# Performance work log

Hardware: AMD Instinct MI355X
Metric: run time of the kernel (lower is better)

Reference implementation:

```python
import jax, jax.numpy as jnp
import numpy as np

T, N, E = 4, 4096, 65536
XD, HD, ZD = 256, 256, 64
EPS = 1e-10


def setup_inputs() -> dict:
    key = jax.random.key(0)
    ks = jax.random.split(key, 30)
    rn = lambda k, sh, s=0.05: jax.random.normal(k, sh, dtype=jnp.float32) * s
    inp = {
        "x": rn(ks[0], (T, N, XD), 1.0),
        "edge_idx": jax.random.randint(ks[1], (T, 2, E), 0, N, dtype=jnp.int32),
        "adj": jax.random.bernoulli(ks[2], 0.005, (T, N, N)).astype(jnp.float32),
        "eps_noise": jax.random.normal(ks[3], (T, N, ZD), dtype=jnp.float32),
        "h0": jnp.zeros((1, N, HD), jnp.float32),
        # phi_x / phi_z (Linear+ReLU)
        "phi_x_w": rn(ks[4], (XD, HD)), "phi_x_b": jnp.zeros((HD,), jnp.float32),
        "phi_z_w": rn(ks[5], (ZD, HD)), "phi_z_b": jnp.zeros((HD,), jnp.float32),
        # encoder GCNs
        "enc_w": rn(ks[6], (2 * HD, HD)), "enc_b": jnp.zeros((HD,), jnp.float32),
        "enc_mean_w": rn(ks[7], (HD, ZD)), "enc_mean_b": jnp.zeros((ZD,), jnp.float32),
        "enc_std_w": rn(ks[8], (HD, ZD)), "enc_std_b": jnp.zeros((ZD,), jnp.float32),
        # prior MLPs
        "prior_w": rn(ks[9], (HD, HD)), "prior_b": jnp.zeros((HD,), jnp.float32),
        "prior_mean_w": rn(ks[10], (HD, ZD)), "prior_mean_b": jnp.zeros((ZD,), jnp.float32),
        "prior_std_w": rn(ks[11], (HD, ZD)), "prior_std_b": jnp.zeros((ZD,), jnp.float32),
        # graph-GRU GCNs (bias=False, n_layers=1; x-input is cat[phi_x, phi_z] -> 2*HD)
        "gru_xz_w": rn(ks[12], (2 * HD, HD)), "gru_hz_w": rn(ks[13], (HD, HD)),
        "gru_xr_w": rn(ks[14], (2 * HD, HD)), "gru_hr_w": rn(ks[15], (HD, HD)),
        "gru_xh_w": rn(ks[16], (2 * HD, HD)), "gru_hh_w": rn(ks[17], (HD, HD)),
    }
    return inp


def _gcn(xf, src, dst, W, b):
    """GCNConv: sym-normalized (A + I) aggregation, then bias. Returns pre-activation."""
    h = xf @ W                                             # [N, out]
    deg = 1.0 + jax.ops.segment_sum(jnp.ones(src.shape[0], xf.dtype), dst, num_segments=N)
    dinv = jax.lax.rsqrt(deg)                              # [N]
    norm = dinv[src] * dinv[dst]                           # [E]
    agg = jax.ops.segment_sum(h[src] * norm[:, None], dst, num_segments=N)
    agg = agg + (dinv * dinv)[:, None] * h                 # self-loop term
    if b is not None:
        agg = agg + b
    return agg


def reference(x, edge_idx, adj, eps_noise, h0,
              phi_x_w, phi_x_b, phi_z_w, phi_z_b,
              enc_w, enc_b, enc_mean_w, enc_mean_b, enc_std_w, enc_std_b,
              prior_w, prior_b, prior_mean_w, prior_mean_b, prior_std_w, prior_std_b,
              gru_xz_w, gru_hz_w, gru_xr_w, gru_hr_w, gru_xh_w, gru_hh_w):
    relu, sp, sig = jax.nn.relu, jax.nn.softplus, jax.nn.sigmoid
    h = h0                                                  # [1, N, HD]
    kld = jnp.float32(0.0)
    nll = jnp.float32(0.0)
    enc_means, prior_means = [], []
    nn_f = jnp.float32(N * N)
    for t in range(T):
        src, dst = edge_idx[t, 0], edge_idx[t, 1]
        phi_x_t = relu(x[t] @ phi_x_w + phi_x_b)                       # [N, HD]
        enc_in = jnp.concatenate([phi_x_t, h[-1]], axis=1)             # [N, 2HD]
        enc_t = relu(_gcn(enc_in, src, dst, enc_w, enc_b))
        enc_mean_t = _gcn(enc_t, src, dst, enc_mean_w, enc_mean_b)     # act = identity
        enc_std_t = sp(_gcn(enc_t, src, dst, enc_std_w, enc_std_b))
        prior_t = relu(h[-1] @ prior_w + prior_b)
        prior_mean_t = prior_t @ prior_mean_w + prior_mean_b
        prior_std_t = sp(prior_t @ prior_std_w + prior_std_b)
        z_t = eps_noise[t] * enc_std_t + enc_mean_t                    # reparameterize
        phi_z_t = relu(z_t @ phi_z_w + phi_z_b)
        dec_t = sig(z_t @ z_t.T)                                       # [N, N] decode
        # graph-GRU step (n_layers = 1, bias=False)
        gin = jnp.concatenate([phi_x_t, phi_z_t], axis=1)              # [N, 2HD]
        z_g = sig(_gcn(gin, src, dst, gru_xz_w, None) + _gcn(h[0], src, dst, gru_hz_w, None))
        r_g = sig(_gcn(gin, src, dst, gru_xr_w, None) + _gcn(h[0], src, dst, gru_hr_w, None))
        h_tilde = jnp.tanh(_gcn(gin, src, dst, gru_xh_w, None)
                           + _gcn(r_g * h[0], src, dst, gru_hh_w, None))
        h = (z_g * h[0] + (1.0 - z_g) * h_tilde)[None]                 # [1, N, HD]
        # KLD (faithful to _kld_gauss, including its sign convention)
        s1, s2 = enc_std_t + EPS, prior_std_t + EPS
        kld_el = (2.0 * jnp.log(s2) - 2.0 * jnp.log(s1)
                  - (s1 * s1 + (enc_mean_t - prior_mean_t) ** 2) / (s2 * s2) + 1.0)
        kld = kld + (0.5 / N) * jnp.mean(jnp.sum(kld_el, axis=0))
        # NLL (faithful quirk: BCE-with-logits applied to sigmoid output dec_t)
        a = adj[t]
        tsum = jnp.sum(a)
        posw = (nn_f - tsum) / tsum
        norm = nn_f / ((nn_f - tsum) * 2.0)
        bce = posw * a * sp(-dec_t) + (1.0 - a) * sp(dec_t)
        nll = nll + norm * jnp.mean(bce)
        enc_means.append(enc_mean_t)
        prior_means.append(prior_mean_t)
    return kld, nll, jnp.stack(enc_means), jnp.stack(prior_means), h
```

## Files before the change

kernel.cpp:

```cpp
#include <hip/hip_runtime.h>
#include <hip/hip_bf16.h>

#define T_STEPS 4
#define N 4096
#define E 65536
#define XD 256
#define HD 256
#define ZD 64

typedef __hip_bfloat16 bf16;
typedef __attribute__((ext_vector_type(8))) short short8;
typedef __attribute__((ext_vector_type(4))) float f32x4;

__device__ __forceinline__ float b2f(bf16 v){ return __bfloat162float(v); }
__device__ __forceinline__ bf16 f2b(float v){ return __float2bfloat16(v); }
__device__ __forceinline__ short f2s(float v){ return __builtin_bit_cast(short, f2b(v)); }
__device__ __forceinline__ float bits2f(unsigned int s){ return __builtin_bit_cast(float, s << 16); }
__device__ __forceinline__ float s2f(short s){ return bits2f((unsigned int)(unsigned short)s); }
__device__ __forceinline__ float splus(float x){ return (x > 15.f) ? x : __logf(1.f + __expf(x)); }
__device__ __forceinline__ float sigm(float x){ return 1.f/(1.f + __expf(-x)); }
__device__ __forceinline__ float ftanh(float x){ return 2.f/(1.f + __expf(-2.f*x)) - 1.f; }

__device__ __forceinline__ float ldI(const void* p, size_t i, int f){
  return f ? ((const float*)p)[i] : b2f(((const bf16*)p)[i]);
}
__device__ __forceinline__ void stO(void* p, size_t i, float v, int f){
  if (f) ((float*)p)[i] = v; else ((bf16*)p)[i] = f2b(v);
}
__device__ __forceinline__ void ld8b(const bf16* p, float v[8]){
  uint4 u = *(const uint4*)p;
  v[0]=bits2f(u.x & 0xffffu); v[1]=bits2f(u.x >> 16);
  v[2]=bits2f(u.y & 0xffffu); v[3]=bits2f(u.y >> 16);
  v[4]=bits2f(u.z & 0xffffu); v[5]=bits2f(u.z >> 16);
  v[6]=bits2f(u.w & 0xffffu); v[7]=bits2f(u.w >> 16);
}
__device__ __forceinline__ void ldW8(const void* W, size_t off, int f, float w[8]){
  if (f == 0){ ld8b((const bf16*)W + off, w); }
  else {
    const float* Wf = (const float*)W + off;
    float4 a = *(const float4*)Wf, b = *(const float4*)(Wf + 4);
    w[0]=a.x; w[1]=a.y; w[2]=a.z; w[3]=a.w; w[4]=b.x; w[5]=b.y; w[6]=b.z; w[7]=b.w;
  }
}
__device__ __forceinline__ unsigned int pack2(float a, float b){
  return (unsigned int)(unsigned short)__builtin_bit_cast(unsigned short, f2b(a))
       | ((unsigned int)(unsigned short)__builtin_bit_cast(unsigned short, f2b(b)) << 16);
}
__device__ __forceinline__ uint4 pack8(const float v[8]){
  uint4 o; o.x = pack2(v[0],v[1]); o.y = pack2(v[2],v[3]);
  o.z = pack2(v[4],v[5]); o.w = pack2(v[6],v[7]);
  return o;
}
__device__ __forceinline__ unsigned int pack2s(short a, short b){
  return (unsigned int)(unsigned short)a | ((unsigned int)(unsigned short)b << 16);
}
__device__ __forceinline__ const void* wofs(const void* W, int f, size_t elems){
  return f ? (const void*)((const float*)W + elems) : (const void*)((const bf16*)W + elems);
}

struct GemmSM { short As[64*72]; short Wt[64*72]; };
struct DecSM  { short Zi[64*72]; short Zj[64*72]; short Adj[64*72];
                float redA[256]; float redB[256]; float redC[256]; };
struct EncSM  { short At[16*264]; short Wt[128*40]; };

struct KP {
  const void *x, *adj, *eps, *h0;
  const int* ei;
  const void *phi_x_w, *phi_x_b, *phi_z_w, *phi_z_b;
  const void *enc_w, *enc_b, *enc_mean_w, *enc_mean_b, *enc_std_w, *enc_std_b;
  const void *prior_w, *prior_b, *prior_mean_w, *prior_mean_b, *prior_std_w, *prior_std_b;
  const void *gxz, *ghz, *gxr, *ghr, *gxh, *ghh;
  void* out;
  float* scal; int* dflag; float* dinv; int* offs; int* srcs; float* enorm; int* deg;
  float* h_prev; bf16* h_bf; bf16* phiXa; bf16* Tb1; bf16* Tb2;
  bf16* zbf; float* z_g; bf16* Gs1; bf16* Gsx; bf16* Gms; bf16* Gh2;
  bf16* PreB;
};

#define OUT_EM ((size_t)2)
#define OUT_PM ((size_t)(2 + (size_t)T_STEPS*N*ZD))
#define OUT_H  ((size_t)(2 + (size_t)2*T_STEPS*N*ZD))

__device__ void mfma_tile(GemmSM& sm, int tid, int f,
    const void* A, int am, int lda, int K,
    const void* W, int ldw, int wcol,
    const void* bias, int act, bf16* C, int ldc, int row0, int ccol0,
    const bf16* pre, int ldpre){
  int ar = tid >> 2, akk = (tid & 3)*16;
  int kp2 = (tid >> 3)*2, wn = (tid & 7)*8;
  int wave = tid >> 6, lane = tid & 63, m = lane & 15, kq = lane >> 4;
  f32x4 acc[4] = {};
  for (int k0 = 0; k0 < K; k0 += 64){
    size_t aidx = (size_t)(row0 + ar)*lda + k0 + akk;
    short8 av0, av1;
    if (am == 2 || f == 0){
      av0 = *(const short8*)((const short*)A + aidx);
      av1 = *(const short8*)((const short*)A + aidx + 8);
    } else {
      const float* Af = (const float*)A + aidx;
      float4 u0 = *(const float4*)(Af);
      float4 u1 = *(const float4*)(Af + 4);
      float4 u2 = *(const float4*)(Af + 8);
      float4 u3 = *(const float4*)(Af + 12);
      av0[0]=f2s(u0.x); av0[1]=f2s(u0.y); av0[2]=f2s(u0.z); av0[3]=f2s(u0.w);
      av0[4]=f2s(u1.x); av0[5]=f2s(u1.y); av0[6]=f2s(u1.z); av0[7]=f2s(u1.w);
      av1[0]=f2s(u2.x); av1[1]=f2s(u2.y); av1[2]=f2s(u2.z); av1[3]=f2s(u2.w);
      av1[4]=f2s(u3.x); av1[5]=f2s(u3.y); av1[6]=f2s(u3.z); av1[7]=f2s(u3.w);
    }
    size_t wi = (size_t)(k0 + kp2)*ldw + wcol + wn;
    short w0[8], w1[8];
    if (f == 0){
      short8 t0 = *(const short8*)((const short*)W + wi);
      short8 t1 = *(const short8*)((const short*)W + wi + ldw);
      #pragma unroll
      for (int j = 0; j < 8; j++){ w0[j] = t0[j]; w1[j] = t1[j]; }
    } else {
      float wf0[8], wf1[8];
      ldW8(W, wi, 1, wf0); ldW8(W, wi + ldw, 1, wf1);
      #pragma unroll
      for (int j = 0; j < 8; j++){ w0[j] = f2s(wf0[j]); w1[j] = f2s(wf1[j]); }
    }
    *(short8*)&sm.As[ar*72 + akk]     = av0;
    *(short8*)&sm.As[ar*72 + akk + 8] = av1;
    #pragma unroll
    for (int j = 0; j < 8; j++){
      int nrow = wn + j;
      int col = (((kp2 >> 3) ^ ((nrow >> 3) & 7)) << 3) | (kp2 & 7);
      *(unsigned int*)&sm.Wt[nrow*72 + col] = pack2s(w0[j], w1[j]);
    }
    __syncthreads();
    short8 afr0 = *(const short8*)&sm.As[(wave*16 + m)*72 + kq*8];
    short8 afr1 = *(const short8*)&sm.As[(wave*16 + m)*72 + (kq + 4)*8];
    #pragma unroll
    for (int t4 = 0; t4 < 4; t4++){
      int nb = t4*16 + m, sb = (nb >> 3) & 7;
      short8 b0 = *(const short8*)&sm.Wt[nb*72 + ((kq ^ sb) << 3)];
      short8 b1 = *(const short8*)&sm.Wt[nb*72 + (((kq + 4) ^ sb) << 3)];
      acc[t4] = __builtin_amdgcn_mfma_f32_16x16x32_bf16(afr0, b0, acc[t4], 0, 0, 0);
      acc[t4] = __builtin_amdgcn_mfma_f32_16x16x32_bf16(afr1, b1, acc[t4], 0, 0, 0);
    }
    __syncthreads();
  }
  #pragma unroll
  for (int t4 = 0; t4 < 4; t4++){
    int c = ccol0 + t4*16 + m;
    float bv = bias ? ldI(bias, wcol + t4*16 + m, f) : 0.f;
    #pragma unroll
    for (int reg = 0; reg < 4; reg++){
      int r = row0 + wave*16 + kq*4 + reg;
      float v = acc[t4][reg] + bv;
      if (pre) v += b2f(pre[(size_t)r*ldpre + t4*16 + m]);
      if (act == 1) v = fmaxf(v, 0.f);
      C[(size_t)r*ldc + c] = f2b(v);
    }
  }
}

__device__ void dec_tile1(const KP& p, DecSM& d, int tid, int t, int u, int f){
  int i0 = (u >> 6)*64, j0 = (u & 63)*64;
  size_t aoff = (size_t)t*N*N;
  #pragma unroll
  for (int i = 0; i < 2; i++){
    int idx = tid + i*256;
    int r = idx >> 3, c = idx & 7;
    int col = ((c ^ ((r >> 3) & 3)) << 3);
    *(short8*)&d.Zi[r*72 + col] = *(const short8*)((const short*)p.zbf + (size_t)(i0+r)*ZD + c*8);
    *(short8*)&d.Zj[r*72 + col] = *(const short8*)((const short*)p.zbf + (size_t)(j0+r)*ZD + c*8);
  }
  {
    int row = tid >> 2, c0 = (tid & 3)*16;
    if (f){
      const float* ap = (const float*)p.adj + aoff + (size_t)(i0+row)*N + j0 + c0;
      short tmp[16];
      #pragma unroll
      for (int q = 0; q < 16; q += 4){
        float4 v = *(const float4*)(ap + q);
        tmp[q]=f2s(v.x); tmp[q+1]=f2s(v.y); tmp[q+2]=f2s(v.z); tmp[q+3]=f2s(v.w);
      }
      *(short8*)&d.Adj[row*72 + c0]     = *(short8*)&tmp[0];
      *(short8*)&d.Adj[row*72 + c0 + 8] = *(short8*)&tmp[8];
    } else {
      const short* ap = (const short*)p.adj + aoff + (size_t)(i0+row)*N + j0 + c0;
      *(short8*)&d.Adj[row*72 + c0]     = *(const short8*)ap;
      *(short8*)&d.Adj[row*72 + c0 + 8] = *(const short8*)(ap + 8);
    }
  }
  __syncthreads();
  int wave = tid >> 6, lane = tid & 63, m = lane & 15, kq = lane >> 4;
  int ra = wave*16 + m, sa = (ra >> 3) & 3;
  short8 a1 = *(const short8*)&d.Zi[ra*72 + ((kq ^ sa) << 3)];
  short8 a2 = *(const short8*)&d.Zi[ra*72 + (((kq+4) ^ sa) << 3)];
  f32x4 acc[4] = {};
  #pragma unroll
  for (int t4 = 0; t4 < 4; t4++){
    int rb = t4*16 + m, sb2 = (rb >> 3) & 3;
    short8 b1 = *(const short8*)&d.Zj[rb*72 + ((kq ^ sb2) << 3)];
    short8 b2 = *(const short8*)&d.Zj[rb*72 + (((kq+4) ^ sb2) << 3)];
    acc[t4] = __builtin_amdgcn_mfma_f32_16x16x32_bf16(a1, b1, acc[t4], 0, 0, 0);
    acc[t4] = __builtin_amdgcn_mfma_f32_16x16x32_bf16(a2, b2, acc[t4], 0, 0, 0);
  }
  float lts = 0.f, lP = 0.f, lQ = 0.f;
  #pragma unroll
  for (int t4 = 0; t4 < 4; t4++){
    int lj = t4*16 + m;
    #pragma unroll
    for (int reg = 0; reg < 4; reg++){
      int li = wave*16 + kq*4 + reg;
      float av = s2f(d.Adj[li*72 + lj]);
      float dec = sigm(acc[t4][reg]);
      lts += av;
      lQ += (1.f - av)*splus(dec);
      if (av != 0.f) lP += av*splus(-dec);
    }
  }
  __syncthreads();
  d.redA[tid] = lts; d.redB[tid] = lP; d.redC[tid] = lQ;
  __syncthreads();
  for (int o = 128; o > 0; o >>= 1){
    if (tid < o){
      d.redA[tid] += d.redA[tid+o];
      d.redB[tid] += d.redB[tid+o];
      d.redC[tid] += d.redC[tid+o];
    }
    __syncthreads();
  }
  if (tid == 0){
    atomicAdd(p.scal + 8 + t,  d.redA[0]);
    atomicAdd(p.scal + 12 + t, d.redB[0]);
    atomicAdd(p.scal + 16 + t, d.redC[0]);
  }
}

__global__ __launch_bounds__(256) void setup0_k(KP p){
  int gb = blockIdx.x, tid = threadIdx.x;
  if (gb == 0){ if (tid < 64) p.scal[tid] = 0.f; }
  else if (gb == 1){
    if (tid == 0){
      const unsigned short* u = (const unsigned short*)p.x;
      int big = 0;
      for (int i = 0; i < 256; i++){ int e = (u[i] >> 7) & 0xFF; if (e >= 134) big++; }
      *p.dflag = (big > 16) ? 1 : 0;
    }
  } else {
    p.deg[(gb-2)*256 + tid] = 0;
  }
}

__global__ __launch_bounds__(256) void count_deg_k(KP p){
  int idx = blockIdx.x*256 + threadIdx.x;
  int t = idx >> 16, e = idx & (E-1);
  int dst = p.ei[(size_t)t*2*E + E + e] & (N-1);
  atomicAdd(&p.deg[t*N + dst], 1);
}

__global__ __launch_bounds__(256) void setup2_k(KP p){
  __shared__ union { int sh[256]; GemmSM g; } sm;
  int gb = blockIdx.x, tid = threadIdx.x;
  int f = *p.dflag;
  if (gb < 4){
    int t = gb;
    const int* dg = p.deg + t*N;
    int* of = p.offs + t*(N+1);
    int base = tid*16;
    int loc[16]; int s = 0;
    #pragma unroll
    for (int i = 0; i < 16; i++){ loc[i] = s; s += dg[base+i]; }
    sm.sh[tid] = s;
    __syncthreads();
    for (int o = 1; o < 256; o <<= 1){
      int v = (tid >= o) ? sm.sh[tid-o] : 0;
      __syncthreads();
      sm.sh[tid] += v;
      __syncthreads();
    }
    int pre = (tid == 0) ? 0 : sm.sh[tid-1];
    #pragma unroll
    for (int i = 0; i < 16; i++){
      int deg_i = dg[base+i];
      of[base+i] = pre + loc[i];
      p.dinv[t*N + base + i] = rsqrtf(1.f + (float)deg_i);
    }
    if (tid == 255) of[N] = sm.sh[255];
    __syncthreads();
    #pragma unroll
    for (int i = 0; i < 16; i++) p.deg[t*N + base + i] = pre + loc[i];
  } else if (gb < 36){
    for (int idx = (gb-4)*256 + tid; idx < N*HD; idx += 32*256){
      float v = ldI(p.h0, idx, f);
      p.h_prev[idx] = v; p.h_bf[idx] = f2b(v);
    }
  } else {
    int u = gb - 36;
    int colblk = u & 3, rowblk = u >> 2;
    mfma_tile(sm.g, tid, f, p.x, 1, XD, XD,
              p.phi_x_w, HD, colblk*64, p.phi_x_b, 1,
              p.phiXa, HD, rowblk*64, colblk*64, nullptr, 0);
  }
}

__global__ __launch_bounds__(256) void setup3_k(KP p){
  __shared__ GemmSM sm;
  int gb = blockIdx.x, tid = threadIdx.x, f = *p.dflag;
  int colblk = gb & 15, rowblk = gb >> 4;
  int grp = colblk >> 2, c4 = colblk & 3;
  const void* W;
  if (grp == 0) W = p.enc_w;
  else if (grp == 1) W = p.gxz;
  else if (grp == 2) W = p.gxr;
  else W = p.gxh;
  mfma_tile(sm, tid, f, p.phiXa, 2, HD, 256,
            W, HD, c4*64, nullptr, 0,
            p.PreB, 1024, rowblk*64, colblk*64, nullptr, 0);
}

__global__ __launch_bounds__(256) void g1_k(KP p, int t){
  __shared__ GemmSM sm;
  int gb = blockIdx.x, tid = threadIdx.x, f = *p.dflag;
  if (gb >= 1024){
    int idx = (gb - 1024)*256 + tid;
    int tt = idx >> 16, e = idx & (E-1);
    int s = p.ei[(size_t)tt*2*E + e] & (N-1);
    int d = p.ei[(size_t)tt*2*E + E + e] & (N-1);
    int pos = atomicAdd(&p.deg[tt*N + d], 1);
    if (pos >= 0 && pos < E){
      p.srcs[(size_t)tt*E + pos] = s;
      p.enorm[(size_t)tt*E + pos] = p.dinv[tt*N + s] * p.dinv[tt*N + d];
    }
    return;
  }
  const bf16* preT = p.PreB + (size_t)t*N*1024;
  int colblk = gb & 15, rowblk = gb >> 4;
  int grp = colblk >> 2, c4 = colblk & 3;
  if (grp == 0)
    mfma_tile(sm, tid, f, p.h_bf, 2, HD, 256,
              wofs(p.enc_w, f, (size_t)256*HD), HD, c4*64, nullptr, 0,
              p.Gs1, 1024, rowblk*64, colblk*64, preT + c4*64, 1024);
  else if (grp == 1)
    mfma_tile(sm, tid, f, p.h_bf, 2, HD, 256,
              p.prior_w, HD, c4*64, p.prior_b, 1,
              p.Gs1, 1024, rowblk*64, colblk*64, nullptr, 0);
  else if (grp == 2)
    mfma_tile(sm, tid, f, p.h_bf, 2, HD, 256,
              p.ghz, HD, c4*64, nullptr, 0,
              p.Gs1, 1024, rowblk*64, colblk*64, nullptr, 0);
  else
    mfma_tile(sm, tid, f, p.h_bf, 2, HD, 256,
              p.ghr, HD, c4*64, nullptr, 0,
              p.Gs1, 1024, rowblk*64, colblk*64, nullptr, 0);
}

__global__ __launch_bounds__(256) void encfused_k(KP p, int t){
  __shared__ union { EncSM e; GemmSM g; } sm;
  int gb = blockIdx.x, tid = threadIdx.x, f = *p.dflag;
  if (gb >= 256){
    int u = gb - 256;
    int colblk = u & 1, rowblk = u >> 1;
    mfma_tile(sm.g, tid, f, p.Gs1 + 256, 2, 1024, 256,
              colblk ? p.prior_std_w : p.prior_mean_w, ZD, 0,
              colblk ? p.prior_std_b : p.prior_mean_b, 0,
              p.Gms, 256, rowblk*64, 128 + colblk*64, nullptr, 0);
    return;
  }
  const int* offs_t = p.offs + t*(N+1);
  const int* srcs_t = p.srcs + (size_t)t*E;
  const float* en_t = p.enorm + (size_t)t*E;
  const float* dv_t = p.dinv + t*N;
  int g16 = tid >> 4, l = tid & 15;
  int n = gb*16 + g16, c = l*16;
  {
    int e0 = offs_t[n], e1 = offs_t[n+1];
    float d2 = dv_t[n]*dv_t[n];
    float acc[16], va[8], vb[8], vc[8], vd[8];
    ld8b(p.Gs1 + (size_t)n*1024 + c, va);
    ld8b(p.Gs1 + (size_t)n*1024 + c + 8, vb);
    #pragma unroll
    for (int j = 0; j < 8; j++){ acc[j] = d2*va[j]; acc[8+j] = d2*vb[j]; }
    int e = e0;
    for (; e + 1 < e1; e += 2){
      int s0 = srcs_t[e] & (N-1), s1 = srcs_t[e+1] & (N-1);
      float n0 = en_t[e], n1 = en_t[e+1];
      ld8b(p.Gs1 + (size_t)s0*1024 + c, va);
      ld8b(p.Gs1 + (size_t)s0*1024 + c + 8, vb);
      ld8b(p.Gs1 + (size_t)s1*1024 + c, vc);
      ld8b(p.Gs1 + (size_t)s1*1024 + c + 8, vd);
      #pragma unroll
      for (int j = 0; j < 8; j++){ acc[j] += n0*va[j] + n1*vc[j]; acc[8+j] += n0*vb[j] + n1*vd[j]; }
    }
    if (e < e1){
      int s0 = srcs_t[e] & (N-1);
      float n0 = en_t[e];
      ld8b(p.Gs1 + (size_t)s0*1024 + c, va);
      ld8b(p.Gs1 + (size_t)s0*1024 + c + 8, vb);
      #pragma unroll
      for (int j = 0; j < 8; j++){ acc[j] += n0*va[j]; acc[8+j] += n0*vb[j]; }
    }
    #pragma unroll
    for (int j = 0; j < 16; j++) acc[j] = fmaxf(acc[j] + ldI(p.enc_b, c + j, f), 0.f);
    *(uint4*)&sm.e.At[g16*264 + c]     = pack8(acc);
    *(uint4*)&sm.e.At[g16*264 + c + 8] = pack8(acc + 8);
  }
  int wave = tid >> 6, lane = tid & 63, m = lane & 15, kq = lane >> 4;
  int kp2e = (tid >> 4)*2;
  int wn2 = (tid & 15)*8;
  f32x4 acc2[2] = {};
  for (int k0 = 0; k0 < 256; k0 += 32){
    const void* Wp = (wn2 < 64) ? p.enc_mean_w : p.enc_std_w;
    int wc = wn2 & 63;
    size_t wi = (size_t)(k0 + kp2e)*ZD + wc;
    short w0[8], w1[8];
    if (f == 0){
      short8 t0 = *(const short8*)((const short*)Wp + wi);
      short8 t1 = *(const short8*)((const short*)Wp + wi + ZD);
      #pragma unroll
      for (int j = 0; j < 8; j++){ w0[j] = t0[j]; w1[j] = t1[j]; }
    } else {
      float wf0[8], wf1[8];
      ldW8(Wp, wi, 1, wf0); ldW8(Wp, wi + ZD, 1, wf1);
      #pragma unroll
      for (int j = 0; j < 8; j++){ w0[j] = f2s(wf0[j]); w1[j] = f2s(wf1[j]); }
    }
    #pragma unroll
    for (int j = 0; j < 8; j++){
      int nrow = wn2 + j;
      int col = (((kp2e >> 3) ^ ((nrow >> 3) & 3)) << 3) | (kp2e & 7);
      *(unsigned int*)&sm.e.Wt[nrow*40 + col] = pack2s(w0[j], w1[j]);
    }
    __syncthreads();
    short8 afr = *(const short8*)&sm.e.At[m*264 + k0 + kq*8];
    #pragma unroll
    for (int t2 = 0; t2 < 2; t2++){
      int nb = wave*32 + t2*16 + m, sb = (nb >> 3) & 3;
      short8 bfr = *(const short8*)&sm.e.Wt[nb*40 + ((kq ^ sb) << 3)];
      acc2[t2] = __builtin_amdgcn_mfma_f32_16x16x32_bf16(afr, bfr, acc2[t2], 0, 0, 0);
    }
    __syncthreads();
  }
  #pragma unroll
  for (int t2 = 0; t2 < 2; t2++){
    int cc = wave*32 + t2*16 + m;
    #pragma unroll
    for (int reg = 0; reg < 4; reg++){
      int node = gb*16 + kq*4 + reg;
      p.Gms[(size_t)node*256 + cc] = f2b(acc2[t2][reg]);
    }
  }
}

__global__ __launch_bounds__(256) void msaggpost_k(KP p, int t){
  __shared__ union { float msh[16*132]; float red[256]; } sm;
  int gb = blockIdx.x, tid = threadIdx.x, f = *p.dflag;
  const int* offs_t = p.offs + t*(N+1);
  const int* srcs_t = p.srcs + (size_t)t*E;
  const float* en_t = p.enorm + (size_t)t*E;
  const float* dv_t = p.dinv + t*N;
  int g16 = tid >> 4, l = tid & 15;
  int n = gb*16 + g16, c = l*8;
  {
    int e0 = offs_t[n], e1 = offs_t[n+1];
    float d2 = dv_t[n]*dv_t[n];
    float acc[8], va[8], vb[8];
    ld8b(p.Gms + (size_t)n*256 + c, va);
    #pragma unroll
    for (int j = 0; j < 8; j++) acc[j] = d2 * va[j];
    int e = e0;
    for (; e + 1 < e1; e += 2){
      int s0 = srcs_t[e] & (N-1), s1 = srcs_t[e+1] & (N-1);
      float n0 = en_t[e], n1 = en_t[e+1];
      ld8b(p.Gms + (size_t)s0*256 + c, va);
      ld8b(p.Gms + (size_t)s1*256 + c, vb);
      #pragma unroll
      for (int j = 0; j < 8; j++) acc[j] += n0*va[j] + n1*vb[j];
    }
    if (e < e1){
      int s0 = srcs_t[e] & (N-1);
      float n0 = en_t[e];
      ld8b(p.Gms + (size_t)s0*256 + c, va);
      #pragma unroll
      for (int j = 0; j < 8; j++) acc[j] += n0*va[j];
    }
    #pragma unroll
    for (int j = 0; j < 8; j++) sm.msh[g16*132 + c + j] = acc[j];
  }
  __syncthreads();
  float el = 0.f;
  {
    int d0 = l*4;
    #pragma unroll
    for (int q = 0; q < 4; q++){
      int d = d0 + q;
      size_t idx = (size_t)n*ZD + d;
      float mean = sm.msh[g16*132 + d] + ldI(p.enc_mean_b, d, f);
      float sd = splus(sm.msh[g16*132 + 64 + d] + ldI(p.enc_std_b, d, f));
      float zv = ldI(p.eps, (size_t)t*N*ZD + idx, f)*sd + mean;
      p.zbf[idx] = f2b(zv);
      stO(p.out, OUT_EM + (size_t)t*N*ZD + idx, mean, f);
      float pm = b2f(p.Gms[(size_t)n*256 + 128 + d]);
      float ps = splus(b2f(p.Gms[(size_t)n*256 + 192 + d]));
      stO(p.out, OUT_PM + (size_t)t*N*ZD + idx, pm, f);
      float s1 = sd + 1e-10f, s2 = ps + 1e-10f;
      float dm = mean - pm;
      el += 2.f*(__logf(s2) - __logf(s1)) - (s1*s1 + dm*dm)/(s2*s2) + 1.f;
    }
  }
  __syncthreads();
  sm.red[tid] = el; __syncthreads();
  for (int o = 128; o > 0; o >>= 1){ if (tid < o) sm.red[tid] += sm.red[tid+o]; __syncthreads(); }
  if (tid == 0) atomicAdd(p.scal + 4, sm.red[0] * (0.5f/((float)N*(float)ZD)));
}

__global__ __launch_bounds__(256) void phiz_k(KP p, int t){
  __shared__ GemmSM sm;
  int gb = blockIdx.x, tid = threadIdx.x, f = *p.dflag;
  int colblk = gb & 3, rowblk = gb >> 2;
  mfma_tile(sm, tid, f, p.zbf, 2, ZD, ZD,
            p.phi_z_w, HD, colblk*64, p.phi_z_b, 1,
            p.Tb2, HD, rowblk*64, colblk*64, nullptr, 0);
}

__global__ __launch_bounds__(256) void grux_dec_k(KP p, int t){
  __shared__ union { GemmSM g; DecSM z; } sm;
  int gb = blockIdx.x, tid = threadIdx.x, f = *p.dflag;
  if (gb < 768){
    int colblk = gb % 12, rowblk = gb / 12;
    int grp = colblk >> 2, c4 = colblk & 3;
    const void* W = (grp == 0) ? p.gxz : ((grp == 1) ? p.gxr : p.gxh);
    mfma_tile(sm.g, tid, f, p.Tb2, 2, HD, 256,
              wofs(W, f, (size_t)256*HD), HD, c4*64, nullptr, 0,
              p.Gsx, 768, rowblk*64, colblk*64,
              p.PreB + (size_t)t*N*1024 + 256 + colblk*64, 1024);
  } else {
    dec_tile1(p, sm.z, tid, t, gb - 768, f);
  }
}

__global__ __launch_bounds__(256) void zr_k(KP p, int t){
  int gb = blockIdx.x, tid = threadIdx.x;
  const int* offs_t = p.offs + t*(N+1);
  const int* srcs_t = p.srcs + (size_t)t*E;
  const float* en_t = p.enorm + (size_t)t*E;
  const float* dv_t = p.dinv + t*N;
  int g4 = tid >> 6, lane = tid & 63;
  int n = gb*4 + g4, c = lane*8;
  int e0 = offs_t[n], e1 = offs_t[n+1];
  float d2 = dv_t[n]*dv_t[n];
  float acc[8], v1[8], v2[8], v3[8], v4[8];
  ld8b(p.Gsx + (size_t)n*768 + c, v1);
  ld8b(p.Gs1 + 512 + (size_t)n*1024 + c, v2);
  #pragma unroll
  for (int j = 0; j < 8; j++) acc[j] = d2 * (v1[j] + v2[j]);
  int e = e0;
  for (; e + 1 < e1; e += 2){
    int s0 = srcs_t[e] & (N-1), s1 = srcs_t[e+1] & (N-1);
    float n0 = en_t[e], n1 = en_t[e+1];
    ld8b(p.Gsx + (size_t)s0*768 + c, v1);
    ld8b(p.Gs1 + 512 + (size_t)s0*1024 + c, v2);
    ld8b(p.Gsx + (size_t)s1*768 + c, v3);
    ld8b(p.Gs1 + 512 + (size_t)s1*1024 + c, v4);
    #pragma unroll
    for (int j = 0; j < 8; j++) acc[j] += n0*(v1[j] + v2[j]) + n1*(v3[j] + v4[j]);
  }
  if (e < e1){
    int s0 = srcs_t[e] & (N-1);
    float n0 = en_t[e];
    ld8b(p.Gsx + (size_t)s0*768 + c, v1);
    ld8b(p.Gs1 + 512 + (size_t)s0*1024 + c, v2);
    #pragma unroll
    for (int j = 0; j < 8; j++) acc[j] += n0*(v1[j] + v2[j]);
  }
  if (c < 256){
    size_t base = (size_t)n*HD + c;
    float4 o0, o1;
    o0.x = sigm(acc[0]); o0.y = sigm(acc[1]); o0.z = sigm(acc[2]); o0.w = sigm(acc[3]);
    o1.x = sigm(acc[4]); o1.y = sigm(acc[5]); o1.z = sigm(acc[6]); o1.w = sigm(acc[7]);
    *(float4*)(p.z_g + base) = o0;
    *(float4*)(p.z_g + base + 4) = o1;
  } else {
    size_t base = (size_t)n*HD + (c - 256);
    float r[8];
    #pragma unroll
    for (int j = 0; j < 8; j++) r[j] = sigm(acc[j]) * p.h_prev[base+j];
    *(uint4*)(p.Tb1 + base) = pack8(r);
  }
}

__global__ __launch_bounds__(256) void hh_k(KP p, int t){
  __shared__ GemmSM sm;
  int gb = blockIdx.x, tid = threadIdx.x, f = *p.dflag;
  int colblk = gb & 3, rowblk = gb >> 2;
  mfma_tile(sm, tid, f, p.Tb1, 2, HD, 256,
            p.ghh, HD, colblk*64, nullptr, 0,
            p.Gh2, 256, rowblk*64, colblk*64, nullptr, 0);
}

__global__ __launch_bounds__(256) void hagg_k(KP p, int t){
  int gb = blockIdx.x, tid = threadIdx.x, f = *p.dflag;
  if (gb >= 512){
    if (tid == 0){
      const float NNf = 16777216.f;
      float nll = 0.f;
      for (int tt = 0; tt < T_STEPS; tt++){
        float ts = p.scal[8+tt], P = p.scal[12+tt], Q = p.scal[16+tt];
        float posw = (NNf - ts)/ts;
        nll += (posw*P + Q) * 0.5f/(NNf - ts);
      }
      stO(p.out, 0, p.scal[4], f);
      stO(p.out, 1, nll, f);
    }
    return;
  }
  const int* offs_t = p.offs + t*(N+1);
  const int* srcs_t = p.srcs + (size_t)t*E;
  const float* en_t = p.enorm + (size_t)t*E;
  const float* dv_t = p.dinv + t*N;
  int g8 = tid >> 5, l = tid & 31;
  int n = gb*8 + g8, c = l*8;
  int e0 = offs_t[n], e1 = offs_t[n+1];
  float d2 = dv_t[n]*dv_t[n];
  float acc[8], v1[8], v2[8], v3[8], v4[8];
  ld8b(p.Gsx + 512 + (size_t)n*768 + c, v1);
  ld8b(p.Gh2 + (size_t)n*256 + c, v2);
  #pragma unroll
  for (int j = 0; j < 8; j++) acc[j] = d2 * (v1[j] + v2[j]);
  int e = e0;
  for (; e + 1 < e1; e += 2){
    int s0 = srcs_t[e] & (N-1), s1 = srcs_t[e+1] & (N-1);
    float n0 = en_t[e], n1 = en_t[e+1];
    ld8b(p.Gsx + 512 + (size_t)s0*768 + c, v1);
    ld8b(p.Gh2 + (size_t)s0*256 + c, v2);
    ld8b(p.Gsx + 512 + (size_t)s1*768 + c, v3);
    ld8b(p.Gh2 + (size_t)s1*256 + c, v4);
    #pragma unroll
    for (int j = 0; j < 8; j++) acc[j] += n0*(v1[j] + v2[j]) + n1*(v3[j] + v4[j]);
  }
  if (e < e1){
    int s0 = srcs_t[e] & (N-1);
    float n0 = en_t[e];
    ld8b(p.Gsx + 512 + (size_t)s0*768 + c, v1);
    ld8b(p.Gh2 + (size_t)s0*256 + c, v2);
    #pragma unroll
    for (int j = 0; j < 8; j++) acc[j] += n0*(v1[j] + v2[j]);
  }
  size_t base = (size_t)n*HD + c;
  #pragma unroll
  for (int j = 0; j < 8; j++){
    float z = p.z_g[base+j];
    float hv = p.h_prev[base+j];
    float nv = z*hv + (1.f - z)*ftanh(acc[j]);
    p.h_prev[base+j] = nv;
    p.h_bf[base+j] = f2b(nv);
    if (t == T_STEPS-1) stO(p.out, OUT_H + base + j, nv, f);
  }
}

extern "C" void kernel_launch(void* const* d_in, const int* in_sizes, int n_in,
                              void* d_out, int out_size, void* d_ws, size_t ws_size,
                              hipStream_t stream){
  KP P;
  P.x = d_in[0];  P.ei = (const int*)d_in[1];  P.adj = d_in[2];  P.eps = d_in[3];  P.h0 = d_in[4];
  P.phi_x_w = d_in[5];  P.phi_x_b = d_in[6];  P.phi_z_w = d_in[7];  P.phi_z_b = d_in[8];
  P.enc_w = d_in[9];  P.enc_b = d_in[10];
  P.enc_mean_w = d_in[11];  P.enc_mean_b = d_in[12];
  P.enc_std_w = d_in[13];   P.enc_std_b = d_in[14];
  P.prior_w = d_in[15];  P.prior_b = d_in[16];
  P.prior_mean_w = d_in[17];  P.prior_mean_b = d_in[18];
  P.prior_std_w = d_in[19];   P.prior_std_b = d_in[20];
  P.gxz = d_in[21];  P.ghz = d_in[22];  P.gxr = d_in[23];
  P.ghr = d_in[24];  P.gxh = d_in[25];  P.ghh = d_in[26];
  P.out = d_out;

  char* wp = (char*)d_ws;
  auto alloc = [&](size_t bytes){ void* q = (void*)wp; wp += (bytes + 255) & ~(size_t)255; return q; };
  P.scal  = (float*)alloc(64*sizeof(float));
  P.dflag = (int*)  alloc(256);
  P.dinv  = (float*)alloc((size_t)T_STEPS*N*4);
  P.offs  = (int*)  alloc((size_t)T_STEPS*(N+1)*4);
  P.srcs  = (int*)  alloc((size_t)T_STEPS*E*4);
  P.enorm = (float*)alloc((size_t)T_STEPS*E*4);
  P.deg   = (int*)  alloc((size_t)T_STEPS*N*4);
  P.h_prev= (float*)alloc((size_t)N*HD*4);
  P.h_bf  = (bf16*) alloc((size_t)N*HD*2);
  P.phiXa = (bf16*) alloc((size_t)T_STEPS*N*HD*2);
  P.Tb1   = (bf16*) alloc((size_t)N*HD*2);
  P.Tb2   = (bf16*) alloc((size_t)N*HD*2);
  P.zbf   = (bf16*) alloc((size_t)N*ZD*2);
  P.z_g   = (float*)alloc((size_t)N*HD*4);
  P.Gs1   = (bf16*) alloc((size_t)N*1024*2);
  P.Gsx   = (bf16*) alloc((size_t)N*768*2);
  P.Gms   = (bf16*) alloc((size_t)N*256*2);
  P.Gh2   = (bf16*) alloc((size_t)N*256*2);
  P.PreB  = (bf16*) alloc((size_t)T_STEPS*N*1024*2);

  setup0_k<<<66,256,0,stream>>>(P);
  count_deg_k<<<1024,256,0,stream>>>(P);
  setup2_k<<<1060,256,0,stream>>>(P);
  setup3_k<<<4096,256,0,stream>>>(P);
  for (int t = 0; t < T_STEPS; t++){
    g1_k<<<(t == 0) ? 2048 : 1024,256,0,stream>>>(P, t);
    encfused_k<<<384,256,0,stream>>>(P, t);
    msaggpost_k<<<256,256,0,stream>>>(P, t);
    phiz_k<<<256,256,0,stream>>>(P, t);
    grux_dec_k<<<4864,256,0,stream>>>(P, t);
    zr_k<<<1024,256,0,stream>>>(P, t);
    hh_k<<<256,256,0,stream>>>(P, t);
    hagg_k<<<(t == T_STEPS-1) ? 513 : 512,256,0,stream>>>(P, t);
  }
}
```

Baseline: 1.311 ms.

## Fuse phi_z GEMM into msaggpost, pre-sum GCN operands before aggregation, use wave-shuffle reductions

Removes the separate phiz_k launch by computing the phi_z linear+ReLU inside msaggpost_k with MFMA, using the z values already staged in shared memory. It also uses GCN linearity to add the h-side GEMM outputs (Gs1 z/r columns, Gsx h column) into the x-side GEMM epilogues, so the zr and hagg aggregation kernels gather one tensor per edge instead of two. The decoder reduction now uses wave shuffles instead of a shared-memory tree. In exchange, each msaggpost block reloads the full phi_z weight into a much larger shared buffer, and intermediate sums are rounded to bf16 once before aggregation.

```diff
diff --git a/kernel.cpp b/kernel.cpp
--- a/kernel.cpp
+++ b/kernel.cpp
@@ -60,7 +60,7 @@
 
 struct GemmSM { short As[64*72]; short Wt[64*72]; };
 struct DecSM  { short Zi[64*72]; short Zj[64*72]; short Adj[64*72];
-                float redA[256]; float redB[256]; float redC[256]; };
+                float redw[12]; };
 struct EncSM  { short At[16*264]; short Wt[128*40]; };
 
 struct KP {
@@ -85,7 +85,7 @@
     const void* A, int am, int lda, int K,
     const void* W, int ldw, int wcol,
     const void* bias, int act, bf16* C, int ldc, int row0, int ccol0,
-    const bf16* pre, int ldpre){
+    const bf16* pre, int ldpre, const bf16* pre2, int ldpre2){
   int ar = tid >> 2, akk = (tid & 3)*16;
   int kp2 = (tid >> 3)*2, wn = (tid & 7)*8;
   int wave = tid >> 6, lane = tid & 63, m = lane & 15, kq = lane >> 4;
@@ -149,7 +149,8 @@
     for (int reg = 0; reg < 4; reg++){
       int r = row0 + wave*16 + kq*4 + reg;
       float v = acc[t4][reg] + bv;
-      if (pre) v += b2f(pre[(size_t)r*ldpre + t4*16 + m]);
+      if (pre)  v += b2f(pre [(size_t)r*ldpre  + t4*16 + m]);
+      if (pre2) v += b2f(pre2[(size_t)r*ldpre2 + t4*16 + m]);
       if (act == 1) v = fmaxf(v, 0.f);
       C[(size_t)r*ldc + c] = f2b(v);
     }
@@ -213,21 +214,18 @@
       if (av != 0.f) lP += av*splus(-dec);
     }
   }
+  #pragma unroll
+  for (int off = 32; off > 0; off >>= 1){
+    lts += __shfl_xor(lts, off);
+    lP  += __shfl_xor(lP,  off);
+    lQ  += __shfl_xor(lQ,  off);
+  }
+  if (lane == 0){ d.redw[wave] = lts; d.redw[4+wave] = lP; d.redw[8+wave] = lQ; }
   __syncthreads();
-  d.redA[tid] = lts; d.redB[tid] = lP; d.redC[tid] = lQ;
-  __syncthreads();
-  for (int o = 128; o > 0; o >>= 1){
-    if (tid < o){
-      d.redA[tid] += d.redA[tid+o];
-      d.redB[tid] += d.redB[tid+o];
-      d.redC[tid] += d.redC[tid+o];
-    }
-    __syncthreads();
-  }
   if (tid == 0){
-    atomicAdd(p.scal + 8 + t,  d.redA[0]);
-    atomicAdd(p.scal + 12 + t, d.redB[0]);
-    atomicAdd(p.scal + 16 + t, d.redC[0]);
+    atomicAdd(p.scal + 8 + t,  d.redw[0]+d.redw[1]+d.redw[2]+d.redw[3]);
+    atomicAdd(p.scal + 12 + t, d.redw[4]+d.redw[5]+d.redw[6]+d.redw[7]);
+    atomicAdd(p.scal + 16 + t, d.redw[8]+d.redw[9]+d.redw[10]+d.redw[11]);
   }
 }
 
@@ -294,7 +292,7 @@
     int colblk = u & 3, rowblk = u >> 2;
     mfma_tile(sm.g, tid, f, p.x, 1, XD, XD,
               p.phi_x_w, HD, colblk*64, p.phi_x_b, 1,
-              p.phiXa, HD, rowblk*64, colblk*64, nullptr, 0);
+              p.phiXa, HD, rowblk*64, colblk*64, nullptr, 0, nullptr, 0);
   }
 }
 
@@ -310,7 +308,7 @@
   else W = p.gxh;
   mfma_tile(sm, tid, f, p.phiXa, 2, HD, 256,
             W, HD, c4*64, nullptr, 0,
-            p.PreB, 1024, rowblk*64, colblk*64, nullptr, 0);
+            p.PreB, 1024, rowblk*64, colblk*64, nullptr, 0, nullptr, 0);
 }
 
 __global__ __launch_bounds__(256) void g1_k(KP p, int t){
@@ -334,19 +332,19 @@
   if (grp == 0)
     mfma_tile(sm, tid, f, p.h_bf, 2, HD, 256,
               wofs(p.enc_w, f, (size_t)256*HD), HD, c4*64, nullptr, 0,
-              p.Gs1, 1024, rowblk*64, colblk*64, preT + c4*64, 1024);
+              p.Gs1, 1024, rowblk*64, colblk*64, preT + c4*64, 1024, nullptr, 0);
   else if (grp == 1)
     mfma_tile(sm, tid, f, p.h_bf, 2, HD, 256,
               p.prior_w, HD, c4*64, p.prior_b, 1,
-              p.Gs1, 1024, rowblk*64, colblk*64, nullptr, 0);
+              p.Gs1, 1024, rowblk*64, colblk*64, nullptr, 0, nullptr, 0);
   else if (grp == 2)
     mfma_tile(sm, tid, f, p.h_bf, 2, HD, 256,
               p.ghz, HD, c4*64, nullptr, 0,
-              p.Gs1, 1024, rowblk*64, colblk*64, nullptr, 0);
+              p.Gs1, 1024, rowblk*64, colblk*64, nullptr, 0, nullptr, 0);
   else
     mfma_tile(sm, tid, f, p.h_bf, 2, HD, 256,
               p.ghr, HD, c4*64, nullptr, 0,
-              p.Gs1, 1024, rowblk*64, colblk*64, nullptr, 0);
+              p.Gs1, 1024, rowblk*64, colblk*64, nullptr, 0, nullptr, 0);
 }
 
 __global__ __launch_bounds__(256) void encfused_k(KP p, int t){
@@ -358,7 +356,7 @@
     mfma_tile(sm.g, tid, f, p.Gs1 + 256, 2, 1024, 256,
               colblk ? p.prior_std_w : p.prior_mean_w, ZD, 0,
               colblk ? p.prior_std_b : p.prior_mean_b, 0,
-              p.Gms, 256, rowblk*64, 128 + colblk*64, nullptr, 0);
+              p.Gms, 256, rowblk*64, 128 + colblk*64, nullptr, 0, nullptr, 0);
     return;
   }
   const int* offs_t = p.offs + t*(N+1);
@@ -447,8 +445,34 @@
 }
 
 __global__ __launch_bounds__(256) void msaggpost_k(KP p, int t){
-  __shared__ union { float msh[16*132]; float red[256]; } sm;
+  __shared__ struct { float msh[16*132]; float red[256];
+                      short zsh[16*72]; short Wt[256*72]; } sm;
   int gb = blockIdx.x, tid = threadIdx.x, f = *p.dflag;
+  {
+    int wn = (tid & 31)*8, kb = (tid >> 5)*2;
+    for (int ko = 0; ko < 64; ko += 16){
+      int kk = kb + ko;
+      short w0[8], w1[8];
+      if (f == 0){
+        short8 t0 = *(const short8*)((const short*)p.phi_z_w + (size_t)kk*HD + wn);
+        short8 t1 = *(const short8*)((const short*)p.phi_z_w + (size_t)(kk+1)*HD + wn);
+        #pragma unroll
+        for (int j = 0; j < 8; j++){ w0[j] = t0[j]; w1[j] = t1[j]; }
+      } else {
+        float a[8], b[8];
+        ldW8(p.phi_z_w, (size_t)kk*HD + wn, 1, a);
+        ldW8(p.phi_z_w, (size_t)(kk+1)*HD + wn, 1, b);
+        #pragma unroll
+        for (int j = 0; j < 8; j++){ w0[j] = f2s(a[j]); w1[j] = f2s(b[j]); }
+      }
+      #pragma unroll
+      for (int j = 0; j < 8; j++){
+        int nrow = wn + j;
+        int pos = (((kk >> 3) ^ ((nrow >> 3) & 7)) << 3) | (kk & 7);
+        *(unsigned int*)&sm.Wt[nrow*72 + pos] = pack2s(w0[j], w1[j]);
+      }
+    }
+  }
   const int* offs_t = p.offs + t*(N+1);
   const int* srcs_t = p.srcs + (size_t)t*E;
   const float* en_t = p.enorm + (size_t)t*E;
@@ -485,6 +509,7 @@
   float el = 0.f;
   {
     int d0 = l*4;
+    float z4[4];
     #pragma unroll
     for (int q = 0; q < 4; q++){
       int d = d0 + q;
@@ -492,6 +517,7 @@
       float mean = sm.msh[g16*132 + d] + ldI(p.enc_mean_b, d, f);
       float sd = splus(sm.msh[g16*132 + 64 + d] + ldI(p.enc_std_b, d, f));
       float zv = ldI(p.eps, (size_t)t*N*ZD + idx, f)*sd + mean;
+      z4[q] = zv;
       p.zbf[idx] = f2b(zv);
       stO(p.out, OUT_EM + (size_t)t*N*ZD + idx, mean, f);
       float pm = b2f(p.Gms[(size_t)n*256 + 128 + d]);
@@ -501,20 +527,37 @@
       float dm = mean - pm;
       el += 2.f*(__logf(s2) - __logf(s1)) - (s1*s1 + dm*dm)/(s2*s2) + 1.f;
     }
-  }
+    *(unsigned int*)&sm.zsh[g16*72 + d0]     = pack2(z4[0], z4[1]);
+    *(unsigned int*)&sm.zsh[g16*72 + d0 + 2] = pack2(z4[2], z4[3]);
+  }
+  sm.red[tid] = el;
   __syncthreads();
-  sm.red[tid] = el; __syncthreads();
+  {
+    int wave = tid >> 6, lane = tid & 63, m = lane & 15, kq = lane >> 4;
+    short8 a0 = *(const short8*)&sm.zsh[m*72 + kq*8];
+    short8 a1 = *(const short8*)&sm.zsh[m*72 + (kq + 4)*8];
+    f32x4 pc[4] = {};
+    #pragma unroll
+    for (int t4 = 0; t4 < 4; t4++){
+      int nb = wave*64 + t4*16 + m, sb = (nb >> 3) & 7;
+      short8 b0 = *(const short8*)&sm.Wt[nb*72 + ((kq ^ sb) << 3)];
+      short8 b1 = *(const short8*)&sm.Wt[nb*72 + (((kq + 4) ^ sb) << 3)];
+      pc[t4] = __builtin_amdgcn_mfma_f32_16x16x32_bf16(a0, b0, pc[t4], 0, 0, 0);
+      pc[t4] = __builtin_amdgcn_mfma_f32_16x16x32_bf16(a1, b1, pc[t4], 0, 0, 0);
+    }
+    #pragma unroll
+    for (int t4 = 0; t4 < 4; t4++){
+      int col = wave*64 + t4*16 + m;
+      float bv = ldI(p.phi_z_b, col, f);
+      #pragma unroll
+      for (int reg = 0; reg < 4; reg++){
+        int node = gb*16 + kq*4 + reg;
+        p.Tb2[(size_t)node*HD + col] = f2b(fmaxf(pc[t4][reg] + bv, 0.f));
+      }
+    }
+  }
   for (int o = 128; o > 0; o >>= 1){ if (tid < o) sm.red[tid] += sm.red[tid+o]; __syncthreads(); }
   if (tid == 0) atomicAdd(p.scal + 4, sm.red[0] * (0.5f/((float)N*(float)ZD)));
-}
-
-__global__ __launch_bounds__(256) void phiz_k(KP p, int t){
-  __shared__ GemmSM sm;
-  int gb = blockIdx.x, tid = threadIdx.x, f = *p.dflag;
-  int colblk = gb & 3, rowblk = gb >> 2;
-  mfma_tile(sm, tid, f, p.zbf, 2, ZD, ZD,
-            p.phi_z_w, HD, colblk*64, p.phi_z_b, 1,
-            p.Tb2, HD, rowblk*64, colblk*64, nullptr, 0);
 }
 
 __global__ __launch_bounds__(256) void grux_dec_k(KP p, int t){
@@ -524,10 +567,13 @@
     int colblk = gb % 12, rowblk = gb / 12;
     int grp = colblk >> 2, c4 = colblk & 3;
     const void* W = (grp == 0) ? p.gxz : ((grp == 1) ? p.gxr : p.gxh);
+    const bf16* pre2 = (grp == 0) ? (p.Gs1 + 512 + c4*64)
+                     : (grp == 1) ? (p.Gs1 + 768 + c4*64) : nullptr;
     mfma_tile(sm.g, tid, f, p.Tb2, 2, HD, 256,
               wofs(W, f, (size_t)256*HD), HD, c4*64, nullptr, 0,
               p.Gsx, 768, rowblk*64, colblk*64,
-              p.PreB + (size_t)t*N*1024 + 256 + colblk*64, 1024);
+              p.PreB + (size_t)t*N*1024 + 256 + colblk*64, 1024,
+              pre2, 1024);
   } else {
     dec_tile1(p, sm.z, tid, t, gb - 768, f);
   }
@@ -543,29 +589,25 @@
   int n = gb*4 + g4, c = lane*8;
   int e0 = offs_t[n], e1 = offs_t[n+1];
   float d2 = dv_t[n]*dv_t[n];
-  float acc[8], v1[8], v2[8], v3[8], v4[8];
+  float acc[8], v1[8], v2[8];
   ld8b(p.Gsx + (size_t)n*768 + c, v1);
-  ld8b(p.Gs1 + 512 + (size_t)n*1024 + c, v2);
-  #pragma unroll
-  for (int j = 0; j < 8; j++) acc[j] = d2 * (v1[j] + v2[j]);
+  #pragma unroll
+  for (int j = 0; j < 8; j++) acc[j] = d2 * v1[j];
   int e = e0;
   for (; e + 1 < e1; e += 2){
     int s0 = srcs_t[e] & (N-1), s1 = srcs_t[e+1] & (N-1);
     float n0 = en_t[e], n1 = en_t[e+1];
     ld8b(p.Gsx + (size_t)s0*768 + c, v1);
-    ld8b(p.Gs1 + 512 + (size_t)s0*1024 + c, v2);
-    ld8b(p.Gsx + (size_t)s1*768 + c, v3);
-    ld8b(p.Gs1 + 512 + (size_t)s1*1024 + c, v4);
-    #pragma unroll
-    for (int j = 0; j < 8; j++) acc[j] += n0*(v1[j] + v2[j]) + n1*(v3[j] + v4[j]);
+    ld8b(p.Gsx + (size_t)s1*768 + c, v2);
+    #pragma unroll
+    for (int j = 0; j < 8; j++) acc[j] += n0*v1[j] + n1*v2[j];
   }
   if (e < e1){
     int s0 = srcs_t[e] & (N-1);
     float n0 = en_t[e];
     ld8b(p.Gsx + (size_t)s0*768 + c, v1);
-    ld8b(p.Gs1 + 512 + (size_t)s0*1024 + c, v2);
-    #pragma unroll
-    for (int j = 0; j < 8; j++) acc[j] += n0*(v1[j] + v2[j]);
+    #pragma unroll
+    for (int j = 0; j < 8; j++) acc[j] += n0*v1[j];
   }
   if (c < 256){
     size_t base = (size_t)n*HD + c;
@@ -589,7 +631,8 @@
   int colblk = gb & 3, rowblk = gb >> 2;
   mfma_tile(sm, tid, f, p.Tb1, 2, HD, 256,
             p.ghh, HD, colblk*64, nullptr, 0,
-            p.Gh2, 256, rowblk*64, colblk*64, nullptr, 0);
+            p.Gh2, 256, rowblk*64, colblk*64, nullptr, 0,
+            p.Gsx + 512 + colblk*64, 768);
 }
 
 __global__ __launch_bounds__(256) void hagg_k(KP p, int t){
@@ -616,29 +659,25 @@
   int n = gb*8 + g8, c = l*8;
   int e0 = offs_t[n], e1 = offs_t[n+1];
   float d2 = dv_t[n]*dv_t[n];
-  float acc[8], v1[8], v2[8], v3[8], v4[8];
-  ld8b(p.Gsx + 512 + (size_t)n*768 + c, v1);
-  ld8b(p.Gh2 + (size_t)n*256 + c, v2);
-  #pragma unroll
-  for (int j = 0; j < 8; j++) acc[j] = d2 * (v1[j] + v2[j]);
+  float acc[8], v1[8], v2[8];
+  ld8b(p.Gh2 + (size_t)n*256 + c, v1);
+  #pragma unroll
+  for (int j = 0; j < 8; j++) acc[j] = d2 * v1[j];
   int e = e0;
   for (; e + 1 < e1; e += 2){
     int s0 = srcs_t[e] & (N-1), s1 = srcs_t[e+1] & (N-1);
     float n0 = en_t[e], n1 = en_t[e+1];
-    ld8b(p.Gsx + 512 + (size_t)s0*768 + c, v1);
-    ld8b(p.Gh2 + (size_t)s0*256 + c, v2);
-    ld8b(p.Gsx + 512 + (size_t)s1*768 + c, v3);
-    ld8b(p.Gh2 + (size_t)s1*256 + c, v4);
-    #pragma unroll
-    for (int j = 0; j < 8; j++) acc[j] += n0*(v1[j] + v2[j]) + n1*(v3[j] + v4[j]);
+    ld8b(p.Gh2 + (size_t)s0*256 + c, v1);
+    ld8b(p.Gh2 + (size_t)s1*256 + c, v2);
+    #pragma unroll
+    for (int j = 0; j < 8; j++) acc[j] += n0*v1[j] + n1*v2[j];
   }
   if (e < e1){
     int s0 = srcs_t[e] & (N-1);
     float n0 = en_t[e];
-    ld8b(p.Gsx + 512 + (size_t)s0*768 + c, v1);
-    ld8b(p.Gh2 + (size_t)s0*256 + c, v2);
-    #pragma unroll
-    for (int j = 0; j < 8; j++) acc[j] += n0*(v1[j] + v2[j]);
+    ld8b(p.Gh2 + (size_t)s0*256 + c, v1);
+    #pragma unroll
+    for (int j = 0; j < 8; j++) acc[j] += n0*v1[j];
   }
   size_t base = (size_t)n*HD + c;
   #pragma unroll
@@ -698,7 +737,6 @@
     g1_k<<<(t == 0) ? 2048 : 1024,256,0,stream>>>(P, t);
     encfused_k<<<384,256,0,stream>>>(P, t);
     msaggpost_k<<<256,256,0,stream>>>(P, t);
-    phiz_k<<<256,256,0,stream>>>(P, t);
     grux_dec_k<<<4864,256,0,stream>>>(P, t);
     zr_k<<<1024,256,0,stream>>>(P, t);
     hh_k<<<256,256,0,stream>>>(P, t);
```

Result: faster. 1.277 ms (-2.5%).
